# Kernel optimization log

Measured on AMD Instinct MI355X. Metric: run time of the kernel, lower is better.

The kernel has to match this reference:

```python
import jax, jax.numpy as jnp
import numpy as np

WS = 7   # window size
SS = 3   # shift size
NH = 8   # num heads
DIM = 256
HH = 56
WW = 56
B = 32


def _layernorm(z, g, b):
    m = z.mean(-1, keepdims=True)
    v = ((z - m) ** 2).mean(-1, keepdims=True)
    return (z - m) / jnp.sqrt(v + 1e-6) * g + b


def _win_partition(z, ws):
    Bd, H, W, C = z.shape
    z = z.reshape(Bd, H // ws, ws, W // ws, ws, C).transpose(0, 1, 3, 2, 4, 5)
    return z.reshape(-1, ws * ws, C)


def _win_reverse(w, ws, Bd, H, W, C):
    w = w.reshape(Bd, H // ws, W // ws, ws, ws, C).transpose(0, 1, 3, 2, 4, 5)
    return w.reshape(Bd, H, W, C)


def _forward(x, attn_mask, rel_pos_index, H, W,
             norm1_g, norm1_b, qkv_w, qkv_b, temperature, rel_table,
             proj_w, proj_b, norm2_g, norm2_b, fc1_w, fc1_b, fc2_w, fc2_b):
    Bd, L, C = x.shape
    hd = C // NH
    N = WS * WS
    shortcut = x
    z = _layernorm(x, norm1_g, norm1_b).reshape(Bd, H, W, C)
    # cyclic shift (H,W divisible by WS -> no padding branch)
    z = jnp.roll(z, (-SS, -SS), axis=(1, 2))
    zw = _win_partition(z, WS)                      # (B*nW, N, C)
    qkv = (zw @ qkv_w + qkv_b).reshape(-1, N, 3, NH, hd).transpose(2, 0, 3, 1, 4)
    q, k, v = qkv[0], qkv[1], qkv[2]                # (B*nW, NH, N, hd)
    attn = jnp.einsum('bhnd,bhmd->bhnm', q, k) * jnp.exp(temperature)
    # LSA diagonal mask (applied BEFORE bias/shift-mask, as in the TF code)
    neg = jnp.finfo(attn.dtype).min
    attn = jnp.where(jnp.eye(N, dtype=bool), neg, attn)
    bias = rel_table[rel_pos_index.reshape(-1)].reshape(N, N, NH).transpose(2, 0, 1)
    attn = attn + bias[None]
    nW = attn_mask.shape[0]
    attn = attn.reshape(Bd, nW, NH, N, N) + attn_mask[None, :, None]
    attn = jax.nn.softmax(attn.reshape(-1, NH, N, N), axis=-1)
    o = jnp.einsum('bhnm,bhmd->bhnd', attn, v).transpose(0, 2, 1, 3).reshape(-1, N, C)
    o = o @ proj_w + proj_b
    o = _win_reverse(o, WS, Bd, H, W, C)
    o = jnp.roll(o, (SS, SS), axis=(1, 2)).reshape(Bd, H * W, C)
    x = shortcut + o
    h = _layernorm(x, norm2_g, norm2_b)
    h = jax.nn.gelu(h @ fc1_w + fc1_b, approximate=False) @ fc2_w + fc2_b
    return x + h


def setup_inputs() -> dict:
    key = jax.random.key(0)
    ks = jax.random.split(key, 8)
    C = DIM
    hd = C // NH
    tn = lambda k, s: jax.random.normal(k, s, jnp.float32) * 0.02
    x = jax.random.normal(ks[0], (B, HH * WW, C), jnp.float32)
    # relative position index (numpy, identical to the TF build())
    coords = np.stack(np.meshgrid(np.arange(WS), np.arange(WS), indexing='ij')).reshape(2, -1)
    rel = (coords[:, :, None] - coords[:, None, :]).transpose(1, 2, 0).astype(np.int64)
    rel[:, :, 0] += WS - 1
    rel[:, :, 1] += WS - 1
    rel[:, :, 0] *= 2 * WS - 1
    rel_pos_index = jnp.asarray(rel.sum(-1), jnp.int32)   # (49,49)
    # shifted-window attention mask (standard Swin construction)
    img_mask = np.zeros((1, HH, WW, 1), np.float32)
    cnt = 0
    for hs in (slice(0, -WS), slice(-WS, -SS), slice(-SS, None)):
        for ws_ in (slice(0, -WS), slice(-WS, -SS), slice(-SS, None)):
            img_mask[:, hs, ws_, :] = cnt
            cnt += 1
    mw = img_mask.reshape(1, HH // WS, WS, WW // WS, WS, 1).transpose(0, 1, 3, 2, 4, 5).reshape(-1, WS * WS)
    am = mw[:, None, :] - mw[:, :, None]
    attn_mask = jnp.asarray(np.where(am != 0, -100.0, 0.0).astype(np.float32))  # (64,49,49)
    return {
        'x': x,
        'attn_mask': attn_mask,
        'norm1_g': jnp.ones((C,), jnp.float32),
        'norm1_b': jnp.zeros((C,), jnp.float32),
        'qkv_w': tn(ks[1], (C, 3 * C)),
        'qkv_b': jnp.zeros((3 * C,), jnp.float32),
        'temperature': jnp.asarray(np.log(hd ** (-0.5)), jnp.float32),
        'rel_table': tn(ks[2], ((2 * WS - 1) ** 2, NH)),
        'proj_w': tn(ks[3], (C, C)),
        'proj_b': jnp.zeros((C,), jnp.float32),
        'norm2_g': jnp.ones((C,), jnp.float32),
        'norm2_b': jnp.zeros((C,), jnp.float32),
        'fc1_w': tn(ks[4], (C, 4 * C)),
        'fc1_b': jnp.zeros((4 * C,), jnp.float32),
        'fc2_w': tn(ks[5], (4 * C, C)),
        'fc2_b': jnp.zeros((C,), jnp.float32),
        'rel_pos_index': rel_pos_index,
        'H': HH,
        'W': WW,
    }


def reference(x, attn_mask, norm1_g, norm1_b, qkv_w, qkv_b, temperature, rel_table,
              proj_w, proj_b, norm2_g, norm2_b, fc1_w, fc1_b, fc2_w, fc2_b,
              rel_pos_index, H, W):
    return _forward(x, attn_mask, rel_pos_index, H, W,
                    norm1_g, norm1_b, qkv_w, qkv_b, temperature, rel_table,
                    proj_w, proj_b, norm2_g, norm2_b, fc1_w, fc1_b, fc2_w, fc2_b)
```

## Files before the change

### kernel.cpp

```cpp
#include <hip/hip_runtime.h>

typedef unsigned short u16;
typedef unsigned int u32;
typedef _Float16 h4 __attribute__((ext_vector_type(4)));
typedef _Float16 h8 __attribute__((ext_vector_type(8)));
typedef float f32x4 __attribute__((ext_vector_type(4)));

#define MFMA16(a, b, c) __builtin_amdgcn_mfma_f32_16x16x32_f16((a), (b), (c), 0, 0, 0)
#define SW(t) ((((t) >> 2) & 3) << 5)

__device__ __forceinline__ float wsum(float v) {
  #pragma unroll
  for (int o = 32; o > 0; o >>= 1) v += __shfl_down(v, o);
  return __shfl(v, 0);
}

__global__ void k_prep_qkv(const float* __restrict__ w, _Float16* __restrict__ o) {
  const int e = blockIdx.x * 256 + threadIdx.x;
  const int r = e >> 8, k = e & 255;
  const int h = r / 96, rem = r - h * 96;
  const int mat = rem >> 5, cc = rem & 31;
  o[e] = (_Float16)w[k * 768 + mat * 256 + h * 32 + cc];
}

__global__ void k_prep_pw(const float* __restrict__ w, _Float16* __restrict__ o) {
  const int e = blockIdx.x * 256 + threadIdx.x;
  const int oc = e >> 8, ic = e & 255;
  o[e] = (_Float16)w[ic * 256 + oc];
}

__global__ void k_prep_w1(const float* __restrict__ w, _Float16* __restrict__ o) {
  const int e = blockIdx.x * 256 + threadIdx.x;
  const int col = e >> 8, k = e & 255;
  o[e] = (_Float16)w[k * 1024 + col];
}

__global__ void k_prep_w2(const float* __restrict__ w, _Float16* __restrict__ o) {
  const int e = blockIdx.x * 256 + threadIdx.x;
  const int oc = e >> 10, k = e & 1023;
  o[e] = (_Float16)w[k * 256 + oc];
}

__global__ void k_prep_btab(const int* __restrict__ rpi, const float* __restrict__ rtab,
                            float* __restrict__ btab) {
  const int e = blockIdx.x * 256 + threadIdx.x;
  if (e < 2401) {
    const int idx = rpi[e];
    #pragma unroll
    for (int h = 0; h < 8; ++h) btab[h * 2401 + e] = rtab[idx * 8 + h];
  }
}

#define X1_OFF 65536
#define MH_OFF 32768

__global__ __launch_bounds__(512, 2) void k_blk(
    const float* __restrict__ x, const _Float16* __restrict__ wsq,
    const _Float16* __restrict__ pwh, const float* __restrict__ qkvb,
    const float* __restrict__ g1, const float* __restrict__ b1,
    const float* __restrict__ temp, const float* __restrict__ btab,
    const float* __restrict__ amask, const float* __restrict__ pb,
    const float* __restrict__ g2, const float* __restrict__ b2,
    const _Float16* __restrict__ w1h, const float* __restrict__ fb1,
    const _Float16* __restrict__ w2h, const float* __restrict__ fb2,
    float* __restrict__ io) {
  __shared__ __align__(16) char smem[131072];
  const int tid = threadIdx.x;
  const int lane = tid & 63, w = tid >> 6;
  const int lr = lane & 15, lk = lane >> 4;
  const int win = blockIdx.x;
  const int bb = win >> 6, wimg = win & 63;
  const int hb = wimg >> 3, wb = wimg & 7;
  const float scale = expf(temp[0]);
  char* const pwv = smem + 32768 + w * 12288;

  {
    const float4 gz = ((const float4*)g1)[lane];
    const float4 bz = ((const float4*)b1)[lane];
    for (int n = w; n < 49; n += 8) {
      int i = n / 7, j = n - 7 * i;
      int rs = hb * 7 + i + 3; if (rs >= 56) rs -= 56;
      int cs = wb * 7 + j + 3; if (cs >= 56) cs -= 56;
      const float4 p = ((const float4*)(x + ((size_t)bb * 3136 + rs * 56 + cs) * 256))[lane];
      float mean = wsum(p.x + p.y + p.z + p.w) * (1.f / 256.f);
      float d0 = p.x - mean, d1 = p.y - mean, d2 = p.z - mean, d3 = p.w - mean;
      float var = wsum(d0 * d0 + d1 * d1 + d2 * d2 + d3 * d3) * (1.f / 256.f);
      float rstd = rsqrtf(var + 1e-6f);
      h4 z;
      z[0] = (_Float16)(d0 * rstd * gz.x + bz.x);
      z[1] = (_Float16)(d1 * rstd * gz.y + bz.y);
      z[2] = (_Float16)(d2 * rstd * gz.z + bz.z);
      z[3] = (_Float16)(d3 * rstd * gz.w + bz.w);
      *(h4*)(smem + ((n * 512 + lane * 8) ^ ((n & 7) << 4))) = z;
    }
  }
  __syncthreads();

  {
    f32x4 zz = {0.f, 0.f, 0.f, 0.f};
    f32x4 acc[4][6];
    #pragma unroll
    for (int t = 0; t < 4; ++t)
      #pragma unroll
      for (int c = 0; c < 6; ++c) acc[t][c] = zz;
    const _Float16* wr[6];
    #pragma unroll
    for (int c = 0; c < 6; ++c)
      wr[c] = wsq + ((size_t)(w * 96 + c * 16 + lr) * 256 + lk * 8);
    const int swzA = (lr & 7) << 4;
    #pragma unroll
    for (int ks = 0; ks < 8; ++ks) {
      const int ko = ks * 64 + lk * 16;
      h8 a[4];
      #pragma unroll
      for (int t = 0; t < 4; ++t)
        a[t] = *(const h8*)(smem + (((t * 16 + lr) * 512 + ko) ^ swzA));
      h8 b[6];
      #pragma unroll
      for (int c = 0; c < 6; ++c) b[c] = *(const h8*)(wr[c] + ks * 32);
      #pragma unroll
      for (int t = 0; t < 4; ++t)
        #pragma unroll
        for (int c = 0; c < 6; ++c) acc[t][c] = MFMA16(a[t], b[c], acc[t][c]);
    }
    #pragma unroll
    for (int c = 0; c < 6; ++c) {
      const int mat = c >> 1;
      const int cc = (c & 1) * 16 + lr;
      const float bias = qkvb[mat * 256 + w * 32 + cc];
      #pragma unroll
      for (int t = 0; t < 4; ++t) {
        const int tok0 = t * 16 + lk * 4;
        if (mat == 2) {
          h4 pk;
          #pragma unroll
          for (int r = 0; r < 4; ++r) {
            float v = (tok0 + r < 49) ? (acc[t][c][r] + bias) : 0.f;
            pk[r] = (_Float16)v;
          }
          *(h4*)(pwv + 8192 + (tok0 >> 3) * 512 + cc * 16 + (tok0 & 7) * 2) = pk;
        } else {
          char* base = pwv + (mat ? 4096 : 0);
          const float mult = mat ? 1.f : scale;
          #pragma unroll
          for (int r = 0; r < 4; ++r) {
            const int tok = tok0 + r;
            float v = (tok < 49) ? (acc[t][c][r] + bias) * mult : 0.f;
            *(_Float16*)(base + ((tok * 64 + cc * 2) ^ (((tok >> 1) & 3) << 4))) = (_Float16)v;
          }
        }
      }
    }
  }
  __syncthreads();

  {
    f32x4 zz = {0.f, 0.f, 0.f, 0.f};
    f32x4 s[4][4];
    #pragma unroll
    for (int t = 0; t < 4; ++t)
      #pragma unroll
      for (int m = 0; m < 4; ++m) s[t][m] = zz;
    const int swzq = ((lr >> 1) & 3) << 4;
    h8 aq[4], bk[4];
    #pragma unroll
    for (int t = 0; t < 4; ++t) {
      aq[t] = *(const h8*)(pwv + (((t * 16 + lr) * 64 + lk * 16) ^ swzq));
      bk[t] = *(const h8*)(pwv + 4096 + (((t * 16 + lr) * 64 + lk * 16) ^ swzq));
    }
    #pragma unroll
    for (int t = 0; t < 4; ++t)
      #pragma unroll
      for (int m = 0; m < 4; ++m) s[t][m] = MFMA16(aq[t], bk[m], s[t][m]);

    const float* bt = btab + (size_t)w * 2401;
    const float* am = amask + (size_t)wimg * 2401;
    #pragma unroll
    for (int t = 0; t < 4; ++t) {
      #pragma unroll
      for (int r = 0; r < 4; ++r) {
        const int n = t * 16 + lk * 4 + r;
        if (n < 49) {
          #pragma unroll
          for (int m = 0; m < 4; ++m) {
            const int mm = m * 16 + lr;
            float sv;
            if (mm >= 49) sv = -1e38f;
            else {
              sv = s[t][m][r];
              if (mm == n) sv = -1e30f;
              const int ee = n * 49 + mm;
              sv += bt[ee] + am[ee];
            }
            s[t][m][r] = sv;
          }
        } else {
          #pragma unroll
          for (int m = 0; m < 4; ++m) s[t][m][r] = 0.f;
        }
      }
    }
    #pragma unroll
    for (int t = 0; t < 4; ++t) {
      #pragma unroll
      for (int r = 0; r < 4; ++r) {
        float mx = fmaxf(fmaxf(s[t][0][r], s[t][1][r]), fmaxf(s[t][2][r], s[t][3][r]));
        mx = fmaxf(mx, __shfl_xor(mx, 1));
        mx = fmaxf(mx, __shfl_xor(mx, 2));
        mx = fmaxf(mx, __shfl_xor(mx, 4));
        mx = fmaxf(mx, __shfl_xor(mx, 8));
        float e0 = expf(s[t][0][r] - mx), e1 = expf(s[t][1][r] - mx);
        float e2 = expf(s[t][2][r] - mx), e3 = expf(s[t][3][r] - mx);
        float sm = e0 + e1 + e2 + e3;
        sm += __shfl_xor(sm, 1);
        sm += __shfl_xor(sm, 2);
        sm += __shfl_xor(sm, 4);
        sm += __shfl_xor(sm, 8);
        const float inv = 1.f / sm;
        const int n = t * 16 + lk * 4 + r;
        const int sw = (n & 7) << 4;
        char* pr = pwv + n * 128;
        *(_Float16*)(pr + ((lr * 2) ^ sw))          = (_Float16)(e0 * inv);
        *(_Float16*)(pr + (((16 + lr) * 2) ^ sw))   = (_Float16)(e1 * inv);
        *(_Float16*)(pr + (((32 + lr) * 2) ^ sw))   = (_Float16)(e2 * inv);
        *(_Float16*)(pr + (((48 + lr) * 2) ^ sw))   = (_Float16)(e3 * inv);
      }
    }
  }

  {
    f32x4 zz = {0.f, 0.f, 0.f, 0.f};
    f32x4 o0[4], o1[4];
    #pragma unroll
    for (int t = 0; t < 4; ++t) { o0[t] = zz; o1[t] = zz; }
    const int swzp = (lr & 7) << 4;
    #pragma unroll
    for (int ks = 0; ks < 2; ++ks) {
      h8 bv0 = *(const h8*)(pwv + 8192 + (ks * 4 + lk) * 512 + lr * 16);
      h8 bv1 = *(const h8*)(pwv + 8192 + (ks * 4 + lk) * 512 + (16 + lr) * 16);
      #pragma unroll
      for (int t = 0; t < 4; ++t) {
        h8 ap = *(const h8*)(pwv + (((t * 16 + lr) * 128 + ks * 64 + lk * 16) ^ swzp));
        o0[t] = MFMA16(ap, bv0, o0[t]);
        o1[t] = MFMA16(ap, bv1, o1[t]);
      }
    }
    #pragma unroll
    for (int t = 0; t < 4; ++t) {
      #pragma unroll
      for (int r = 0; r < 4; ++r) {
        const int tok = t * 16 + lk * 4 + r;
        const int sw = (tok & 7) << 4;
        char* orow = smem + tok * 512;
        *(_Float16*)(orow + (((w * 32 + lr) * 2) ^ sw))      = (_Float16)o0[t][r];
        *(_Float16*)(orow + (((w * 32 + 16 + lr) * 2) ^ sw)) = (_Float16)o1[t][r];
      }
    }
  }
  __syncthreads();

  {
    f32x4 zz = {0.f, 0.f, 0.f, 0.f};
    f32x4 oacc[4][2];
    #pragma unroll
    for (int t = 0; t < 4; ++t) { oacc[t][0] = zz; oacc[t][1] = zz; }
    const int swzA = (lr & 7) << 4;
    const _Float16* pwr = pwh + (size_t)(w * 32 + lr) * 256 + lk * 8;
    #pragma unroll
    for (int ks = 0; ks < 8; ++ks) {
      const int ko = ks * 64 + lk * 16;
      h8 b0 = *(const h8*)(pwr + ks * 32);
      h8 b1 = *(const h8*)(pwr + 16 * 256 + ks * 32);
      #pragma unroll
      for (int t = 0; t < 4; ++t) {
        h8 a = *(const h8*)(smem + (((t * 16 + lr) * 512 + ko) ^ swzA));
        oacc[t][0] = MFMA16(a, b0, oacc[t][0]);
        oacc[t][1] = MFMA16(a, b1, oacc[t][1]);
      }
    }
    const float pb0 = pb[w * 32 + lr];
    const float pb1 = pb[w * 32 + 16 + lr];
    #pragma unroll
    for (int t = 0; t < 4; ++t) {
      #pragma unroll
      for (int r = 0; r < 4; ++r) {
        const int tok = t * 16 + lk * 4 + r;
        float v0 = 0.f, v1 = 0.f;
        if (tok < 49) {
          const int i = tok / 7, j = tok - 7 * i;
          int rs = hb * 7 + i + 3; if (rs >= 56) rs -= 56;
          int cs = wb * 7 + j + 3; if (cs >= 56) cs -= 56;
          const size_t ro = ((size_t)bb * 3136 + rs * 56 + cs) * 256 + w * 32 + lr;
          v0 = x[ro]      + oacc[t][0][r] + pb0;
          v1 = x[ro + 16] + oacc[t][1][r] + pb1;
        }
        char* xr = smem + X1_OFF + tok * 1024;
        *(float*)(xr + (((w * 32 + lr) * 4)      ^ SW(tok))) = v0;
        *(float*)(xr + (((w * 32 + 16 + lr) * 4) ^ SW(tok))) = v1;
      }
    }
  }
  __syncthreads();

  {
    const float4 gz = ((const float4*)g2)[lane];
    const float4 bz = ((const float4*)b2)[lane];
    for (int n = w; n < 64; n += 8) {
      const float4 p = *(const float4*)(smem + X1_OFF + n * 1024 + ((lane * 16) ^ SW(n)));
      float mean = wsum(p.x + p.y + p.z + p.w) * (1.f / 256.f);
      float d0 = p.x - mean, d1 = p.y - mean, d2 = p.z - mean, d3 = p.w - mean;
      float var = wsum(d0 * d0 + d1 * d1 + d2 * d2 + d3 * d3) * (1.f / 256.f);
      float rstd = rsqrtf(var + 1e-6f);
      h4 z;
      z[0] = (_Float16)(d0 * rstd * gz.x + bz.x);
      z[1] = (_Float16)(d1 * rstd * gz.y + bz.y);
      z[2] = (_Float16)(d2 * rstd * gz.z + bz.z);
      z[3] = (_Float16)(d3 * rstd * gz.w + bz.w);
      *(h4*)(smem + ((n * 512 + lane * 8) ^ ((n & 7) << 4))) = z;
    }
  }
  __syncthreads();

  f32x4 zzm = {0.f, 0.f, 0.f, 0.f};
  f32x4 macc[4][2];
  #pragma unroll
  for (int t = 0; t < 4; ++t) { macc[t][0] = zzm; macc[t][1] = zzm; }
  const int swz = (lr & 7) << 4;

  for (int ch = 0; ch < 4; ++ch) {
    f32x4 facc[4][2];
    #pragma unroll
    for (int t = 0; t < 4; ++t) { facc[t][0] = zzm; facc[t][1] = zzm; }
    {
      const _Float16* w1p = w1h + (size_t)(ch * 256 + w * 32 + lr) * 256 + lk * 8;
      #pragma unroll
      for (int ks = 0; ks < 8; ++ks) {
        const int ko = ks * 64 + lk * 16;
        h8 b0 = *(const h8*)(w1p + ks * 32);
        h8 b1 = *(const h8*)(w1p + 16 * 256 + ks * 32);
        #pragma unroll
        for (int t = 0; t < 4; ++t) {
          h8 a = *(const h8*)(smem + (((t * 16 + lr) * 512 + ko) ^ swz));
          facc[t][0] = MFMA16(a, b0, facc[t][0]);
          facc[t][1] = MFMA16(a, b1, facc[t][1]);
        }
      }
    }
    #pragma unroll
    for (int nt = 0; nt < 2; ++nt) {
      const float bb2 = fb1[ch * 256 + w * 32 + nt * 16 + lr];
      #pragma unroll
      for (int t = 0; t < 4; ++t) {
        #pragma unroll
        for (int r = 0; r < 4; ++r) {
          float a = facc[t][nt][r] + bb2;
          float gl = 0.5f * a * (1.f + erff(a * 0.70710678118654752f));
          const int tok = t * 16 + lk * 4 + r;
          *(_Float16*)(smem + MH_OFF +
                       ((tok * 512 + w * 64 + nt * 32 + lr * 2) ^ ((tok & 7) << 4))) =
              (_Float16)gl;
        }
      }
    }
    __syncthreads();
    {
      const _Float16* w2p = w2h + (size_t)(w * 32 + lr) * 1024 + ch * 256 + lk * 8;
      #pragma unroll
      for (int ks = 0; ks < 8; ++ks) {
        const int ko = ks * 64 + lk * 16;
        h8 b0 = *(const h8*)(w2p + ks * 32);
        h8 b1 = *(const h8*)(w2p + 16 * 1024 + ks * 32);
        #pragma unroll
        for (int t = 0; t < 4; ++t) {
          h8 a = *(const h8*)(smem + MH_OFF + (((t * 16 + lr) * 512 + ko) ^ swz));
          macc[t][0] = MFMA16(a, b0, macc[t][0]);
          macc[t][1] = MFMA16(a, b1, macc[t][1]);
        }
      }
    }
    __syncthreads();
  }

  {
    const float bv0 = fb2[w * 32 + lr];
    const float bv1 = fb2[w * 32 + 16 + lr];
    #pragma unroll
    for (int t = 0; t < 4; ++t) {
      #pragma unroll
      for (int r = 0; r < 4; ++r) {
        const int tok = t * 16 + lk * 4 + r;
        char* xr = smem + X1_OFF + tok * 1024;
        float* p0 = (float*)(xr + (((w * 32 + lr) * 4)      ^ SW(tok)));
        float* p1 = (float*)(xr + (((w * 32 + 16 + lr) * 4) ^ SW(tok)));
        *p0 += macc[t][0][r] + bv0;
        *p1 += macc[t][1][r] + bv1;
      }
    }
  }
  __syncthreads();

  for (int n = w; n < 49; n += 8) {
    const int i = n / 7, j = n - 7 * i;
    int rs = hb * 7 + i + 3; if (rs >= 56) rs -= 56;
    int cs = wb * 7 + j + 3; if (cs >= 56) cs -= 56;
    const float4 v = *(const float4*)(smem + X1_OFF + n * 1024 + ((lane * 16) ^ SW(n)));
    *(float4*)(io + ((size_t)bb * 3136 + rs * 56 + cs) * 256 + lane * 4) = v;
  }
}

extern "C" void kernel_launch(void* const* d_in, const int* in_sizes, int n_in,
                              void* d_out, int out_size, void* d_ws, size_t ws_size,
                              hipStream_t stream) {
  const float* x     = (const float*)d_in[0];
  const float* amask = (const float*)d_in[1];
  const float* g1    = (const float*)d_in[2];
  const float* b1    = (const float*)d_in[3];
  const float* qkvw  = (const float*)d_in[4];
  const float* qkvb  = (const float*)d_in[5];
  const float* temp  = (const float*)d_in[6];
  const float* rtab  = (const float*)d_in[7];
  const float* pw    = (const float*)d_in[8];
  const float* pb    = (const float*)d_in[9];
  const float* g2    = (const float*)d_in[10];
  const float* b2    = (const float*)d_in[11];
  const float* w1    = (const float*)d_in[12];
  const float* fb1   = (const float*)d_in[13];
  const float* w2    = (const float*)d_in[14];
  const float* fb2   = (const float*)d_in[15];
  const int* rpi     = (const int*)d_in[16];

  char* ws = (char*)d_ws;
  _Float16* wsq = (_Float16*)ws;
  _Float16* pwh = (_Float16*)(ws + 393216);
  _Float16* w1h = (_Float16*)(ws + 524288);
  _Float16* w2h = (_Float16*)(ws + 1048576);
  float* btab   = (float*)(ws + 1572864);
  float* io = (float*)d_out;

  k_prep_qkv<<<768, 256, 0, stream>>>(qkvw, wsq);
  k_prep_pw<<<256, 256, 0, stream>>>(pw, pwh);
  k_prep_w1<<<1024, 256, 0, stream>>>(w1, w1h);
  k_prep_w2<<<1024, 256, 0, stream>>>(w2, w2h);
  k_prep_btab<<<10, 256, 0, stream>>>(rpi, rtab, btab);
  k_blk<<<2048, 512, 0, stream>>>(x, wsq, pwh, qkvb, g1, b1, temp, btab,
                                  amask, pb, g2, b2, w1h, fb1, w2h, fb2, io);
}
```

Measured before the change: 843.1 us.

## Halve block to four waves with two heads per wave and fp16 residual buffer

After: 1.057 ms. +25.4%, slower.

```diff
diff --git a/kernel.cpp b/kernel.cpp
--- a/kernel.cpp
+++ b/kernel.cpp
@@ -7,7 +7,6 @@
 typedef float f32x4 __attribute__((ext_vector_type(4)));
 
 #define MFMA16(a, b, c) __builtin_amdgcn_mfma_f32_16x16x32_f16((a), (b), (c), 0, 0, 0)
-#define SW(t) ((((t) >> 2) & 3) << 5)
 
 __device__ __forceinline__ float wsum(float v) {
   #pragma unroll
@@ -51,10 +50,10 @@
   }
 }
 
-#define X1_OFF 65536
-#define MH_OFF 32768
-
-__global__ __launch_bounds__(512, 2) void k_blk(
+#define X1_OFF 32768
+#define H_OFF  65536
+
+__global__ __launch_bounds__(256, 2) void k_blk(
     const float* __restrict__ x, const _Float16* __restrict__ wsq,
     const _Float16* __restrict__ pwh, const float* __restrict__ qkvb,
     const float* __restrict__ g1, const float* __restrict__ b1,
@@ -64,7 +63,7 @@
     const _Float16* __restrict__ w1h, const float* __restrict__ fb1,
     const _Float16* __restrict__ w2h, const float* __restrict__ fb2,
     float* __restrict__ io) {
-  __shared__ __align__(16) char smem[131072];
+  __shared__ __align__(16) char smem[81920];
   const int tid = threadIdx.x;
   const int lane = tid & 63, w = tid >> 6;
   const int lr = lane & 15, lk = lane >> 4;
@@ -77,7 +76,7 @@
   {
     const float4 gz = ((const float4*)g1)[lane];
     const float4 bz = ((const float4*)b1)[lane];
-    for (int n = w; n < 49; n += 8) {
+    for (int n = w; n < 49; n += 4) {
       int i = n / 7, j = n - 7 * i;
       int rs = hb * 7 + i + 3; if (rs >= 56) rs -= 56;
       int cs = wb * 7 + j + 3; if (cs >= 56) cs -= 56;
@@ -96,207 +95,225 @@
   }
   __syncthreads();
 
+  f32x4 oA0[4], oA1[4], oB0[4], oB1[4];
+
+  auto do_head = [&](const int h, f32x4 (&po0)[4], f32x4 (&po1)[4]) {
+    f32x4 zz = {0.f, 0.f, 0.f, 0.f};
+    {
+      f32x4 acc[4][6];
+      #pragma unroll
+      for (int t = 0; t < 4; ++t)
+        #pragma unroll
+        for (int c = 0; c < 6; ++c) acc[t][c] = zz;
+      const _Float16* wr[6];
+      #pragma unroll
+      for (int c = 0; c < 6; ++c)
+        wr[c] = wsq + ((size_t)(h * 96 + c * 16 + lr) * 256 + lk * 8);
+      const int swzA = (lr & 7) << 4;
+      #pragma unroll
+      for (int ks = 0; ks < 8; ++ks) {
+        const int ko = ks * 64 + lk * 16;
+        h8 a[4];
+        #pragma unroll
+        for (int t = 0; t < 4; ++t)
+          a[t] = *(const h8*)(smem + (((t * 16 + lr) * 512 + ko) ^ swzA));
+        h8 b[6];
+        #pragma unroll
+        for (int c = 0; c < 6; ++c) b[c] = *(const h8*)(wr[c] + ks * 32);
+        #pragma unroll
+        for (int t = 0; t < 4; ++t)
+          #pragma unroll
+          for (int c = 0; c < 6; ++c) acc[t][c] = MFMA16(a[t], b[c], acc[t][c]);
+      }
+      #pragma unroll
+      for (int c = 0; c < 6; ++c) {
+        const int mat = c >> 1;
+        const int cc = (c & 1) * 16 + lr;
+        const float bias = qkvb[mat * 256 + h * 32 + cc];
+        #pragma unroll
+        for (int t = 0; t < 4; ++t) {
+          const int tok0 = t * 16 + lk * 4;
+          if (mat == 2) {
+            h4 pk;
+            #pragma unroll
+            for (int r = 0; r < 4; ++r) {
+              float v = (tok0 + r < 49) ? (acc[t][c][r] + bias) : 0.f;
+              pk[r] = (_Float16)v;
+            }
+            *(h4*)(pwv + 8192 + (tok0 >> 3) * 512 + cc * 16 + (tok0 & 7) * 2) = pk;
+          } else {
+            char* base = pwv + (mat ? 4096 : 0);
+            const float mult = mat ? 1.f : scale;
+            #pragma unroll
+            for (int r = 0; r < 4; ++r) {
+              const int tok = tok0 + r;
+              float v = (tok < 49) ? (acc[t][c][r] + bias) * mult : 0.f;
+              *(_Float16*)(base + ((tok * 64 + cc * 2) ^ (((tok >> 1) & 3) << 4))) = (_Float16)v;
+            }
+          }
+        }
+      }
+    }
+    {
+      f32x4 s[4][4];
+      #pragma unroll
+      for (int t = 0; t < 4; ++t)
+        #pragma unroll
+        for (int m = 0; m < 4; ++m) s[t][m] = zz;
+      const int swzq = ((lr >> 1) & 3) << 4;
+      h8 aq[4], bk[4];
+      #pragma unroll
+      for (int t = 0; t < 4; ++t) {
+        aq[t] = *(const h8*)(pwv + (((t * 16 + lr) * 64 + lk * 16) ^ swzq));
+        bk[t] = *(const h8*)(pwv + 4096 + (((t * 16 + lr) * 64 + lk * 16) ^ swzq));
+      }
+      #pragma unroll
+      for (int t = 0; t < 4; ++t)
+        #pragma unroll
+        for (int m = 0; m < 4; ++m) s[t][m] = MFMA16(aq[t], bk[m], s[t][m]);
+
+      const float* bt = btab + (size_t)h * 2401;
+      const float* am = amask + (size_t)wimg * 2401;
+      #pragma unroll
+      for (int t = 0; t < 4; ++t) {
+        #pragma unroll
+        for (int r = 0; r < 4; ++r) {
+          const int n = t * 16 + lk * 4 + r;
+          if (n < 49) {
+            #pragma unroll
+            for (int m = 0; m < 4; ++m) {
+              const int mm = m * 16 + lr;
+              float sv;
+              if (mm >= 49) sv = -1e38f;
+              else {
+                sv = s[t][m][r];
+                if (mm == n) sv = -1e30f;
+                const int ee = n * 49 + mm;
+                sv += bt[ee] + am[ee];
+              }
+              s[t][m][r] = sv;
+            }
+          } else {
+            #pragma unroll
+            for (int m = 0; m < 4; ++m) s[t][m][r] = 0.f;
+          }
+        }
+      }
+      #pragma unroll
+      for (int t = 0; t < 4; ++t) {
+        #pragma unroll
+        for (int r = 0; r < 4; ++r) {
+          float mx = fmaxf(fmaxf(s[t][0][r], s[t][1][r]), fmaxf(s[t][2][r], s[t][3][r]));
+          mx = fmaxf(mx, __shfl_xor(mx, 1));
+          mx = fmaxf(mx, __shfl_xor(mx, 2));
+          mx = fmaxf(mx, __shfl_xor(mx, 4));
+          mx = fmaxf(mx, __shfl_xor(mx, 8));
+          float e0 = expf(s[t][0][r] - mx), e1 = expf(s[t][1][r] - mx);
+          float e2 = expf(s[t][2][r] - mx), e3 = expf(s[t][3][r] - mx);
+          float sm = e0 + e1 + e2 + e3;
+          sm += __shfl_xor(sm, 1);
+          sm += __shfl_xor(sm, 2);
+          sm += __shfl_xor(sm, 4);
+          sm += __shfl_xor(sm, 8);
+          const float inv = 1.f / sm;
+          const int n = t * 16 + lk * 4 + r;
+          const int sw = (n & 7) << 4;
+          char* pr = pwv + n * 128;
+          *(_Float16*)(pr + ((lr * 2) ^ sw))        = (_Float16)(e0 * inv);
+          *(_Float16*)(pr + (((16 + lr) * 2) ^ sw)) = (_Float16)(e1 * inv);
+          *(_Float16*)(pr + (((32 + lr) * 2) ^ sw)) = (_Float16)(e2 * inv);
+          *(_Float16*)(pr + (((48 + lr) * 2) ^ sw)) = (_Float16)(e3 * inv);
+        }
+      }
+    }
+    {
+      #pragma unroll
+      for (int t = 0; t < 4; ++t) { po0[t] = zz; po1[t] = zz; }
+      const int swzp = (lr & 7) << 4;
+      #pragma unroll
+      for (int ks = 0; ks < 2; ++ks) {
+        h8 bv0 = *(const h8*)(pwv + 8192 + (ks * 4 + lk) * 512 + lr * 16);
+        h8 bv1 = *(const h8*)(pwv + 8192 + (ks * 4 + lk) * 512 + (16 + lr) * 16);
+        #pragma unroll
+        for (int t = 0; t < 4; ++t) {
+          h8 ap = *(const h8*)(pwv + (((t * 16 + lr) * 128 + ks * 64 + lk * 16) ^ swzp));
+          po0[t] = MFMA16(ap, bv0, po0[t]);
+          po1[t] = MFMA16(ap, bv1, po1[t]);
+        }
+      }
+    }
+  };
+
+  do_head(w, oA0, oA1);
+  do_head(w + 4, oB0, oB1);
+  __syncthreads();
+
+  {
+    auto write_o = [&](const int h, f32x4 (&po0)[4], f32x4 (&po1)[4]) {
+      #pragma unroll
+      for (int t = 0; t < 4; ++t) {
+        #pragma unroll
+        for (int r = 0; r < 4; ++r) {
+          const int tok = t * 16 + lk * 4 + r;
+          const int sw = (tok & 7) << 4;
+          char* orow = smem + tok * 512;
+          *(_Float16*)(orow + (((h * 32 + lr) * 2) ^ sw))      = (_Float16)po0[t][r];
+          *(_Float16*)(orow + (((h * 32 + 16 + lr) * 2) ^ sw)) = (_Float16)po1[t][r];
+        }
+      }
+    };
+    write_o(w, oA0, oA1);
+    write_o(w + 4, oB0, oB1);
+  }
+  __syncthreads();
+
   {
     f32x4 zz = {0.f, 0.f, 0.f, 0.f};
-    f32x4 acc[4][6];
+    f32x4 pacc[4][4];
     #pragma unroll
     for (int t = 0; t < 4; ++t)
       #pragma unroll
-      for (int c = 0; c < 6; ++c) acc[t][c] = zz;
-    const _Float16* wr[6];
-    #pragma unroll
-    for (int c = 0; c < 6; ++c)
-      wr[c] = wsq + ((size_t)(w * 96 + c * 16 + lr) * 256 + lk * 8);
+      for (int n = 0; n < 4; ++n) pacc[t][n] = zz;
     const int swzA = (lr & 7) << 4;
+    const _Float16* pwr = pwh + (size_t)(w * 64 + lr) * 256 + lk * 8;
     #pragma unroll
     for (int ks = 0; ks < 8; ++ks) {
       const int ko = ks * 64 + lk * 16;
-      h8 a[4];
-      #pragma unroll
-      for (int t = 0; t < 4; ++t)
-        a[t] = *(const h8*)(smem + (((t * 16 + lr) * 512 + ko) ^ swzA));
-      h8 b[6];
-      #pragma unroll
-      for (int c = 0; c < 6; ++c) b[c] = *(const h8*)(wr[c] + ks * 32);
-      #pragma unroll
-      for (int t = 0; t < 4; ++t)
-        #pragma unroll
-        for (int c = 0; c < 6; ++c) acc[t][c] = MFMA16(a[t], b[c], acc[t][c]);
-    }
-    #pragma unroll
-    for (int c = 0; c < 6; ++c) {
-      const int mat = c >> 1;
-      const int cc = (c & 1) * 16 + lr;
-      const float bias = qkvb[mat * 256 + w * 32 + cc];
-      #pragma unroll
-      for (int t = 0; t < 4; ++t) {
-        const int tok0 = t * 16 + lk * 4;
-        if (mat == 2) {
-          h4 pk;
-          #pragma unroll
-          for (int r = 0; r < 4; ++r) {
-            float v = (tok0 + r < 49) ? (acc[t][c][r] + bias) : 0.f;
-            pk[r] = (_Float16)v;
-          }
-          *(h4*)(pwv + 8192 + (tok0 >> 3) * 512 + cc * 16 + (tok0 & 7) * 2) = pk;
-        } else {
-          char* base = pwv + (mat ? 4096 : 0);
-          const float mult = mat ? 1.f : scale;
-          #pragma unroll
-          for (int r = 0; r < 4; ++r) {
-            const int tok = tok0 + r;
-            float v = (tok < 49) ? (acc[t][c][r] + bias) * mult : 0.f;
-            *(_Float16*)(base + ((tok * 64 + cc * 2) ^ (((tok >> 1) & 3) << 4))) = (_Float16)v;
-          }
-        }
-      }
-    }
-  }
-  __syncthreads();
-
-  {
-    f32x4 zz = {0.f, 0.f, 0.f, 0.f};
-    f32x4 s[4][4];
-    #pragma unroll
-    for (int t = 0; t < 4; ++t)
-      #pragma unroll
-      for (int m = 0; m < 4; ++m) s[t][m] = zz;
-    const int swzq = ((lr >> 1) & 3) << 4;
-    h8 aq[4], bk[4];
-    #pragma unroll
-    for (int t = 0; t < 4; ++t) {
-      aq[t] = *(const h8*)(pwv + (((t * 16 + lr) * 64 + lk * 16) ^ swzq));
-      bk[t] = *(const h8*)(pwv + 4096 + (((t * 16 + lr) * 64 + lk * 16) ^ swzq));
-    }
-    #pragma unroll
-    for (int t = 0; t < 4; ++t)
-      #pragma unroll
-      for (int m = 0; m < 4; ++m) s[t][m] = MFMA16(aq[t], bk[m], s[t][m]);
-
-    const float* bt = btab + (size_t)w * 2401;
-    const float* am = amask + (size_t)wimg * 2401;
-    #pragma unroll
-    for (int t = 0; t < 4; ++t) {
-      #pragma unroll
-      for (int r = 0; r < 4; ++r) {
-        const int n = t * 16 + lk * 4 + r;
-        if (n < 49) {
-          #pragma unroll
-          for (int m = 0; m < 4; ++m) {
-            const int mm = m * 16 + lr;
-            float sv;
-            if (mm >= 49) sv = -1e38f;
-            else {
-              sv = s[t][m][r];
-              if (mm == n) sv = -1e30f;
-              const int ee = n * 49 + mm;
-              sv += bt[ee] + am[ee];
-            }
-            s[t][m][r] = sv;
-          }
-        } else {
-          #pragma unroll
-          for (int m = 0; m < 4; ++m) s[t][m][r] = 0.f;
-        }
-      }
-    }
-    #pragma unroll
-    for (int t = 0; t < 4; ++t) {
-      #pragma unroll
-      for (int r = 0; r < 4; ++r) {
-        float mx = fmaxf(fmaxf(s[t][0][r], s[t][1][r]), fmaxf(s[t][2][r], s[t][3][r]));
-        mx = fmaxf(mx, __shfl_xor(mx, 1));
-        mx = fmaxf(mx, __shfl_xor(mx, 2));
-        mx = fmaxf(mx, __shfl_xor(mx, 4));
-        mx = fmaxf(mx, __shfl_xor(mx, 8));
-        float e0 = expf(s[t][0][r] - mx), e1 = expf(s[t][1][r] - mx);
-        float e2 = expf(s[t][2][r] - mx), e3 = expf(s[t][3][r] - mx);
-        float sm = e0 + e1 + e2 + e3;
-        sm += __shfl_xor(sm, 1);
-        sm += __shfl_xor(sm, 2);
-        sm += __shfl_xor(sm, 4);
-        sm += __shfl_xor(sm, 8);
-        const float inv = 1.f / sm;
-        const int n = t * 16 + lk * 4 + r;
-        const int sw = (n & 7) << 4;
-        char* pr = pwv + n * 128;
-        *(_Float16*)(pr + ((lr * 2) ^ sw))          = (_Float16)(e0 * inv);
-        *(_Float16*)(pr + (((16 + lr) * 2) ^ sw))   = (_Float16)(e1 * inv);
-        *(_Float16*)(pr + (((32 + lr) * 2) ^ sw))   = (_Float16)(e2 * inv);
-        *(_Float16*)(pr + (((48 + lr) * 2) ^ sw))   = (_Float16)(e3 * inv);
-      }
-    }
-  }
-
-  {
-    f32x4 zz = {0.f, 0.f, 0.f, 0.f};
-    f32x4 o0[4], o1[4];
-    #pragma unroll
-    for (int t = 0; t < 4; ++t) { o0[t] = zz; o1[t] = zz; }
-    const int swzp = (lr & 7) << 4;
-    #pragma unroll
-    for (int ks = 0; ks < 2; ++ks) {
-      h8 bv0 = *(const h8*)(pwv + 8192 + (ks * 4 + lk) * 512 + lr * 16);
-      h8 bv1 = *(const h8*)(pwv + 8192 + (ks * 4 + lk) * 512 + (16 + lr) * 16);
-      #pragma unroll
-      for (int t = 0; t < 4; ++t) {
-        h8 ap = *(const h8*)(pwv + (((t * 16 + lr) * 128 + ks * 64 + lk * 16) ^ swzp));
-        o0[t] = MFMA16(ap, bv0, o0[t]);
-        o1[t] = MFMA16(ap, bv1, o1[t]);
-      }
-    }
+      h8 b[4];
+      #pragma unroll
+      for (int nt = 0; nt < 4; ++nt) b[nt] = *(const h8*)(pwr + nt * 16 * 256 + ks * 32);
+      #pragma unroll
+      for (int t = 0; t < 4; ++t) {
+        h8 a = *(const h8*)(smem + (((t * 16 + lr) * 512 + ko) ^ swzA));
+        #pragma unroll
+        for (int nt = 0; nt < 4; ++nt) pacc[t][nt] = MFMA16(a, b[nt], pacc[t][nt]);
+      }
+    }
+    float pbv[4];
+    #pragma unroll
+    for (int nt = 0; nt < 4; ++nt) pbv[nt] = pb[w * 64 + nt * 16 + lr];
     #pragma unroll
     for (int t = 0; t < 4; ++t) {
       #pragma unroll
       for (int r = 0; r < 4; ++r) {
         const int tok = t * 16 + lk * 4 + r;
         const int sw = (tok & 7) << 4;
-        char* orow = smem + tok * 512;
-        *(_Float16*)(orow + (((w * 32 + lr) * 2) ^ sw))      = (_Float16)o0[t][r];
-        *(_Float16*)(orow + (((w * 32 + 16 + lr) * 2) ^ sw)) = (_Float16)o1[t][r];
-      }
-    }
-  }
-  __syncthreads();
-
-  {
-    f32x4 zz = {0.f, 0.f, 0.f, 0.f};
-    f32x4 oacc[4][2];
-    #pragma unroll
-    for (int t = 0; t < 4; ++t) { oacc[t][0] = zz; oacc[t][1] = zz; }
-    const int swzA = (lr & 7) << 4;
-    const _Float16* pwr = pwh + (size_t)(w * 32 + lr) * 256 + lk * 8;
-    #pragma unroll
-    for (int ks = 0; ks < 8; ++ks) {
-      const int ko = ks * 64 + lk * 16;
-      h8 b0 = *(const h8*)(pwr + ks * 32);
-      h8 b1 = *(const h8*)(pwr + 16 * 256 + ks * 32);
-      #pragma unroll
-      for (int t = 0; t < 4; ++t) {
-        h8 a = *(const h8*)(smem + (((t * 16 + lr) * 512 + ko) ^ swzA));
-        oacc[t][0] = MFMA16(a, b0, oacc[t][0]);
-        oacc[t][1] = MFMA16(a, b1, oacc[t][1]);
-      }
-    }
-    const float pb0 = pb[w * 32 + lr];
-    const float pb1 = pb[w * 32 + 16 + lr];
-    #pragma unroll
-    for (int t = 0; t < 4; ++t) {
-      #pragma unroll
-      for (int r = 0; r < 4; ++r) {
-        const int tok = t * 16 + lk * 4 + r;
-        float v0 = 0.f, v1 = 0.f;
+        char* xr = smem + X1_OFF + tok * 512;
         if (tok < 49) {
           const int i = tok / 7, j = tok - 7 * i;
           int rs = hb * 7 + i + 3; if (rs >= 56) rs -= 56;
           int cs = wb * 7 + j + 3; if (cs >= 56) cs -= 56;
-          const size_t ro = ((size_t)bb * 3136 + rs * 56 + cs) * 256 + w * 32 + lr;
-          v0 = x[ro]      + oacc[t][0][r] + pb0;
-          v1 = x[ro + 16] + oacc[t][1][r] + pb1;
-        }
-        char* xr = smem + X1_OFF + tok * 1024;
-        *(float*)(xr + (((w * 32 + lr) * 4)      ^ SW(tok))) = v0;
-        *(float*)(xr + (((w * 32 + 16 + lr) * 4) ^ SW(tok))) = v1;
+          const size_t ro = ((size_t)bb * 3136 + rs * 56 + cs) * 256 + w * 64 + lr;
+          #pragma unroll
+          for (int nt = 0; nt < 4; ++nt) {
+            float v = x[ro + nt * 16] + pacc[t][nt][r] + pbv[nt];
+            *(_Float16*)(xr + (((w * 64 + nt * 16 + lr) * 2) ^ sw)) = (_Float16)v;
+          }
+        } else {
+          #pragma unroll
+          for (int nt = 0; nt < 4; ++nt)
+            *(_Float16*)(xr + (((w * 64 + nt * 16 + lr) * 2) ^ sw)) = (_Float16)0.f;
+        }
       }
     }
   }
@@ -305,10 +322,11 @@
   {
     const float4 gz = ((const float4*)g2)[lane];
     const float4 bz = ((const float4*)b2)[lane];
-    for (int n = w; n < 64; n += 8) {
-      const float4 p = *(const float4*)(smem + X1_OFF + n * 1024 + ((lane * 16) ^ SW(n)));
-      float mean = wsum(p.x + p.y + p.z + p.w) * (1.f / 256.f);
-      float d0 = p.x - mean, d1 = p.y - mean, d2 = p.z - mean, d3 = p.w - mean;
+    for (int n = w; n < 64; n += 4) {
+      const h4 ph = *(const h4*)(smem + ((X1_OFF + n * 512 + lane * 8) ^ ((n & 7) << 4)));
+      float p0 = (float)ph[0], p1 = (float)ph[1], p2 = (float)ph[2], p3 = (float)ph[3];
+      float mean = wsum(p0 + p1 + p2 + p3) * (1.f / 256.f);
+      float d0 = p0 - mean, d1 = p1 - mean, d2 = p2 - mean, d3 = p3 - mean;
       float var = wsum(d0 * d0 + d1 * d1 + d2 * d2 + d3 * d3) * (1.f / 256.f);
       float rstd = rsqrtf(var + 1e-6f);
       h4 z;
@@ -322,17 +340,19 @@
   __syncthreads();
 
   f32x4 zzm = {0.f, 0.f, 0.f, 0.f};
-  f32x4 macc[4][2];
+  f32x4 macc[4][4];
   #pragma unroll
-  for (int t = 0; t < 4; ++t) { macc[t][0] = zzm; macc[t][1] = zzm; }
+  for (int t = 0; t < 4; ++t)
+    #pragma unroll
+    for (int n = 0; n < 4; ++n) macc[t][n] = zzm;
   const int swz = (lr & 7) << 4;
 
-  for (int ch = 0; ch < 4; ++ch) {
+  for (int ch = 0; ch < 8; ++ch) {
     f32x4 facc[4][2];
     #pragma unroll
     for (int t = 0; t < 4; ++t) { facc[t][0] = zzm; facc[t][1] = zzm; }
     {
-      const _Float16* w1p = w1h + (size_t)(ch * 256 + w * 32 + lr) * 256 + lk * 8;
+      const _Float16* w1p = w1h + (size_t)(ch * 128 + w * 32 + lr) * 256 + lk * 8;
       #pragma unroll
       for (int ks = 0; ks < 8; ++ks) {
         const int ko = ks * 64 + lk * 16;
@@ -348,7 +368,7 @@
     }
     #pragma unroll
     for (int nt = 0; nt < 2; ++nt) {
-      const float bb2 = fb1[ch * 256 + w * 32 + nt * 16 + lr];
+      const float bb2 = fb1[ch * 128 + w * 32 + nt * 16 + lr];
       #pragma unroll
       for (int t = 0; t < 4; ++t) {
         #pragma unroll
@@ -356,25 +376,27 @@
           float a = facc[t][nt][r] + bb2;
           float gl = 0.5f * a * (1.f + erff(a * 0.70710678118654752f));
           const int tok = t * 16 + lk * 4 + r;
-          *(_Float16*)(smem + MH_OFF +
-                       ((tok * 512 + w * 64 + nt * 32 + lr * 2) ^ ((tok & 7) << 4))) =
+          *(_Float16*)(smem + H_OFF +
+                       ((tok * 256 + (w * 32 + nt * 16 + lr) * 2) ^ ((tok & 15) << 4))) =
               (_Float16)gl;
         }
       }
     }
     __syncthreads();
     {
-      const _Float16* w2p = w2h + (size_t)(w * 32 + lr) * 1024 + ch * 256 + lk * 8;
-      #pragma unroll
-      for (int ks = 0; ks < 8; ++ks) {
+      const _Float16* w2p = w2h + (size_t)(w * 64 + lr) * 1024 + ch * 128 + lk * 8;
+      #pragma unroll
+      for (int ks = 0; ks < 4; ++ks) {
         const int ko = ks * 64 + lk * 16;
-        h8 b0 = *(const h8*)(w2p + ks * 32);
-        h8 b1 = *(const h8*)(w2p + 16 * 1024 + ks * 32);
+        h8 b[4];
+        #pragma unroll
+        for (int nt = 0; nt < 4; ++nt) b[nt] = *(const h8*)(w2p + nt * 16 * 1024 + ks * 32);
         #pragma unroll
         for (int t = 0; t < 4; ++t) {
-          h8 a = *(const h8*)(smem + MH_OFF + (((t * 16 + lr) * 512 + ko) ^ swz));
-          macc[t][0] = MFMA16(a, b0, macc[t][0]);
-          macc[t][1] = MFMA16(a, b1, macc[t][1]);
+          h8 a = *(const h8*)(smem + H_OFF +
+                              (((t * 16 + lr) * 256 + ko) ^ (((t * 16 + lr) & 15) << 4)));
+          #pragma unroll
+          for (int nt = 0; nt < 4; ++nt) macc[t][nt] = MFMA16(a, b[nt], macc[t][nt]);
         }
       }
     }
@@ -382,29 +404,29 @@
   }
 
   {
-    const float bv0 = fb2[w * 32 + lr];
-    const float bv1 = fb2[w * 32 + 16 + lr];
+    float bv[4];
+    #pragma unroll
+    for (int nt = 0; nt < 4; ++nt) bv[nt] = fb2[w * 64 + nt * 16 + lr];
     #pragma unroll
     for (int t = 0; t < 4; ++t) {
       #pragma unroll
       for (int r = 0; r < 4; ++r) {
         const int tok = t * 16 + lk * 4 + r;
-        char* xr = smem + X1_OFF + tok * 1024;
-        float* p0 = (float*)(xr + (((w * 32 + lr) * 4)      ^ SW(tok)));
-        float* p1 = (float*)(xr + (((w * 32 + 16 + lr) * 4) ^ SW(tok)));
-        *p0 += macc[t][0][r] + bv0;
-        *p1 += macc[t][1][r] + bv1;
-      }
-    }
-  }
-  __syncthreads();
-
-  for (int n = w; n < 49; n += 8) {
-    const int i = n / 7, j = n - 7 * i;
-    int rs = hb * 7 + i + 3; if (rs >= 56) rs -= 56;
-    int cs = wb * 7 + j + 3; if (cs >= 56) cs -= 56;
-    const float4 v = *(const float4*)(smem + X1_OFF + n * 1024 + ((lane * 16) ^ SW(n)));
-    *(float4*)(io + ((size_t)bb * 3136 + rs * 56 + cs) * 256 + lane * 4) = v;
+        if (tok < 49) {
+          const int i = tok / 7, j = tok - 7 * i;
+          int rs = hb * 7 + i + 3; if (rs >= 56) rs -= 56;
+          int cs = wb * 7 + j + 3; if (cs >= 56) cs -= 56;
+          const size_t ro = ((size_t)bb * 3136 + rs * 56 + cs) * 256 + w * 64 + lr;
+          const int sw = (tok & 7) << 4;
+          const char* xr = smem + X1_OFF + tok * 512;
+          #pragma unroll
+          for (int nt = 0; nt < 4; ++nt) {
+            float x1v = (float)(*(const _Float16*)(xr + (((w * 64 + nt * 16 + lr) * 2) ^ sw)));
+            io[ro + nt * 16] = x1v + macc[t][nt][r] + bv[nt];
+          }
+        }
+      }
+    }
   }
 }
 
@@ -442,6 +464,6 @@
   k_prep_w1<<<1024, 256, 0, stream>>>(w1, w1h);
   k_prep_w2<<<1024, 256, 0, stream>>>(w2, w2h);
   k_prep_btab<<<10, 256, 0, stream>>>(rpi, rtab, btab);
-  k_blk<<<2048, 512, 0, stream>>>(x, wsq, pwh, qkvb, g1, b1, temp, btab,
+  k_blk<<<2048, 256, 0, stream>>>(x, wsq, pwh, qkvb, g1, b1, temp, btab,
                                   amask, pb, g2, b2, w1h, fb1, w2h, fb2, io);
 }
```
